# Kernel optimization log

Measured on AMD Instinct MI355X. Metric: run time of the kernel, lower is better.

Reference implementation:

```python
import jax, jax.numpy as jnp
import numpy as np

B, L, H = 4, 1024, 1024
NH, HD = 16, 64
ND = NH * HD
ITERS = 4
U = 5  # MSA1 ring window size (hard-coded in source)


def _conv1x1(w, b, x):  # w [O,C], b [O], x [B,C,L] -> [B,O,L]  (Conv2d 1x1 == per-position linear)
    return jnp.einsum('oc,bcl->bol', w, x) + b[None, :, None]


def _layernorm(x, s, b, eps=1e-5):  # x [B,H,L]; LayerNorm over channel dim H
    mu = x.mean(1, keepdims=True)
    var = ((x - mu) ** 2).mean(1, keepdims=True)
    return (x - mu) / jnp.sqrt(var + eps) * s[None, :, None] + b[None, :, None]


def _msa1(x, ax, wq, bq, wk, bk, wv, bv, wo, bo):
    # x [B,H,L] normalized nodes; ax [B,H,2,L] (ring embedding + relay)
    b, h, l = x.shape
    q = _conv1x1(wq, bq, x).reshape(b, NH, HD, l)
    k = _conv1x1(wk, bk, x).reshape(b, NH, HD, l)
    v = _conv1x1(wv, bv, x).reshape(b, NH, HD, l)
    pad = U // 2
    kp = jnp.pad(k, ((0, 0), (0, 0), (0, 0), (pad, pad)))
    vp = jnp.pad(v, ((0, 0), (0, 0), (0, 0), (pad, pad)))
    # F.unfold with (U,1) kernel along L == stack of U shifted views
    kw = jnp.stack([kp[..., u:u + l] for u in range(U)], axis=3)  # [B,NH,HD,U,L]
    vw = jnp.stack([vp[..., u:u + l] for u in range(U)], axis=3)
    al = ax.shape[2]
    ak = (jnp.einsum('oc,bcal->boal', wk, ax) + bk[None, :, None, None]).reshape(b, NH, HD, al, l)
    av = (jnp.einsum('oc,bcal->boal', wv, ax) + bv[None, :, None, None]).reshape(b, NH, HD, al, l)
    kw = jnp.concatenate([kw, ak], axis=3)  # [B,NH,HD,U+2,L]
    vw = jnp.concatenate([vw, av], axis=3)
    scores = (q[:, :, :, None, :] * kw).sum(2) / np.sqrt(HD)  # [B,NH,U+2,L]
    alphas = jax.nn.softmax(scores, axis=2)
    att = (alphas[:, :, None, :, :] * vw).sum(3).reshape(b, ND, l)
    return _conv1x1(wo, bo, att)  # [B,H,L]


def _msa2(relay, y, smask, wq, bq, wk, bk, wo, bo):
    # relay [B,H]; y [B,H,L+1]; smask [B,L+1] True at padding
    b = relay.shape[0]
    q = (jnp.einsum('oc,bc->bo', wq, relay) + bq).reshape(b, NH, HD)
    k = _conv1x1(wk, bk, y).reshape(b, NH, HD, -1)
    pre = jnp.einsum('bnd,bndl->bnl', q, k) / np.sqrt(HD)
    pre = jnp.where(smask[:, None, :], -1e10, pre)
    alphas = jax.nn.softmax(pre, axis=-1)
    # NOTE: source has v = k (WV output unused) -- reproduced faithfully
    att = jnp.einsum('bnl,bndl->bnd', alphas, k).reshape(b, ND)
    return jnp.einsum('oc,bc->bo', wo, att) + bo  # [B,H]


def _star_forward(data, mask, ln_s, ln_b, rwq, rwq_b, rwk, rwk_b, rwv, rwv_b, rwo, rwo_b,
                  swq, swq_b, swk, swk_b, swo, swo_b):
    b, l, h = data.shape
    pad_mask = (mask == 0)  # True at padding positions
    smask = jnp.concatenate([jnp.zeros((b, 1), bool), pad_mask], axis=1)  # [B,L+1]
    embs = jnp.transpose(data, (0, 2, 1))  # [B,H,L]
    nodes = embs
    relay = embs.mean(2)  # [B,H]
    for i in range(ITERS):
        xn = _layernorm(nodes, ln_s[i], ln_b[i])
        ax = jnp.stack([embs, jnp.broadcast_to(relay[:, :, None], embs.shape)], axis=2)  # [B,H,2,L]
        ring = _msa1(xn, ax, rwq[i], rwq_b[i], rwk[i], rwk_b[i], rwv[i], rwv_b[i], rwo[i], rwo_b[i])
        nodes = nodes + jax.nn.leaky_relu(ring)
        y = jnp.concatenate([relay[:, :, None], nodes], axis=2)  # [B,H,L+1]
        relay = jax.nn.leaky_relu(_msa2(relay, y, smask, swq[i], swq_b[i], swk[i], swk_b[i], swo[i], swo_b[i]))
        nodes = jnp.where(pad_mask[:, None, :], 0.0, nodes)
    return jnp.transpose(nodes, (0, 2, 1)), relay  # [B,L,H], [B,H]


def setup_inputs() -> dict:
    key = jax.random.key(0)
    ks = jax.random.split(key, 16)
    def p(k, shape):
        return jax.random.normal(k, shape, jnp.float32) * 0.02
    return dict(
        data=jax.random.normal(ks[0], (B, L, H), jnp.float32),
        mask=jax.random.randint(ks[1], (B, L), 0, 2).astype(jnp.int32),
        ln_s=jnp.ones((ITERS, H), jnp.float32),
        ln_b=jnp.zeros((ITERS, H), jnp.float32),
        rwq=p(ks[2], (ITERS, ND, H)), rwq_b=p(ks[3], (ITERS, ND)),
        rwk=p(ks[4], (ITERS, ND, H)), rwk_b=p(ks[5], (ITERS, ND)),
        rwv=p(ks[6], (ITERS, ND, H)), rwv_b=p(ks[7], (ITERS, ND)),
        rwo=p(ks[8], (ITERS, H, ND)), rwo_b=p(ks[9], (ITERS, H)),
        swq=p(ks[10], (ITERS, ND, H)), swq_b=p(ks[11], (ITERS, ND)),
        swk=p(ks[12], (ITERS, ND, H)), swk_b=p(ks[13], (ITERS, ND)),
        swo=p(ks[14], (ITERS, H, ND)), swo_b=p(ks[15], (ITERS, H)),
    )


def reference(data, mask, ln_s, ln_b, rwq, rwq_b, rwk, rwk_b, rwv, rwv_b, rwo, rwo_b,
              swq, swq_b, swk, swk_b, swo, swo_b):
    return _star_forward(data, mask, ln_s, ln_b, rwq, rwq_b, rwk, rwk_b, rwv, rwv_b,
                         rwo, rwo_b, swq, swq_b, swk, swk_b, swo, swo_b)
```

## Files before the change

kernel.cpp:

```cpp
#include <hip/hip_runtime.h>
#include <math.h>

namespace {

constexpr int B_ = 4, L_ = 1024, H_ = 1024, NH_ = 16, HD_ = 64, ND_ = 1024, ITERS_ = 4;

typedef unsigned short u16;
typedef __attribute__((ext_vector_type(8))) short short8;
typedef __attribute__((ext_vector_type(4))) float f32x4;

__device__ inline u16 f2bf(float f) {
  unsigned u = __builtin_bit_cast(unsigned, f);
  u += 0x7FFFu + ((u >> 16) & 1u);
  return (u16)(u >> 16);
}
__device__ inline float bf2f(u16 v) {
  unsigned u = ((unsigned)v) << 16;
  return __builtin_bit_cast(float, u);
}

__device__ inline void gl_lds16(const u16* g, u16* l) {
  __builtin_amdgcn_global_load_lds((const __attribute__((address_space(1))) void*)g,
                                   (__attribute__((address_space(3))) void*)l, 16, 0, 0);
}

__global__ void k_prep(const float* __restrict__ data, const float* __restrict__ rwq,
                       const float* __restrict__ rwk, const float* __restrict__ rwv,
                       const float* __restrict__ rwo, const float* __restrict__ swk,
                       u16* __restrict__ embs_bf, u16* __restrict__ wq_bf,
                       u16* __restrict__ wk_bf, u16* __restrict__ wv_bf,
                       u16* __restrict__ wo_bf, u16* __restrict__ swk_bf,
                       float* __restrict__ nodes) {
  int i = blockIdx.x * 256 + threadIdx.x;
  int which = blockIdx.y;
  if (which == 6) {
    reinterpret_cast<float4*>(nodes)[i] = reinterpret_cast<const float4*>(data)[i];
    return;
  }
  const float* src;
  u16* dst;
  switch (which) {
    case 0: src = data; dst = embs_bf; break;
    case 1: src = rwq; dst = wq_bf; break;
    case 2: src = rwk; dst = wk_bf; break;
    case 3: src = rwv; dst = wv_bf; break;
    case 4: src = rwo; dst = wo_bf; break;
    default: src = swk; dst = swk_bf; break;
  }
  float4 v = reinterpret_cast<const float4*>(src)[i];
  ushort4 o;
  o.x = f2bf(v.x); o.y = f2bf(v.y); o.z = f2bf(v.z); o.w = f2bf(v.w);
  reinterpret_cast<ushort4*>(dst)[i] = o;
}

__global__ void k_relay_part(const float* __restrict__ data, float* __restrict__ part) {
  int b = blockIdx.z, chunk = blockIdx.y;
  int c = blockIdx.x * 256 + threadIdx.x;
  const float* p = data + ((size_t)b * L_ + chunk * 128) * H_ + c;
  float acc = 0.f;
  for (int l = 0; l < 128; ++l) acc += p[(size_t)l * H_];
  part[((size_t)b * 8 + chunk) * H_ + c] = acc;
}
__global__ void k_relay_reduce(const float* __restrict__ part, float* __restrict__ relay) {
  int i = blockIdx.x * 256 + threadIdx.x;
  int b = i >> 10, c = i & 1023;
  float acc = 0.f;
  for (int j = 0; j < 8; ++j) acc += part[((size_t)b * 8 + j) * H_ + c];
  relay[i] = acc * (1.f / (float)L_);
}

__global__ __launch_bounds__(256) void k_layernorm_bf(float* __restrict__ nodes,
                                                      const float* __restrict__ s,
                                                      const float* __restrict__ bb,
                                                      const int* __restrict__ mask,
                                                      u16* __restrict__ y, int do_zero) {
  int row = blockIdx.x * 4 + (threadIdx.x >> 6);
  int lane = threadIdx.x & 63;
  int b = row >> 10, l = row & 1023;
  bool pad = do_zero && (mask[b * L_ + l] == 0);
  float4* xr = reinterpret_cast<float4*>(nodes + (size_t)row * H_);
  float4 v[4];
  float sum = 0.f, sq = 0.f;
#pragma unroll
  for (int j = 0; j < 4; ++j) {
    v[j] = pad ? float4{0.f, 0.f, 0.f, 0.f} : xr[lane + 64 * j];
    sum += v[j].x + v[j].y + v[j].z + v[j].w;
    sq += v[j].x * v[j].x + v[j].y * v[j].y + v[j].z * v[j].z + v[j].w * v[j].w;
  }
  if (pad) {
#pragma unroll
    for (int j = 0; j < 4; ++j) xr[lane + 64 * j] = float4{0.f, 0.f, 0.f, 0.f};
  }
#pragma unroll
  for (int off = 32; off; off >>= 1) {
    sum += __shfl_xor(sum, off);
    sq += __shfl_xor(sq, off);
  }
  float mu = sum * (1.f / (float)H_);
  float rstd = rsqrtf(sq * (1.f / (float)H_) - mu * mu + 1e-5f);
  ushort4* yr = reinterpret_cast<ushort4*>(y + (size_t)row * H_);
#pragma unroll
  for (int j = 0; j < 4; ++j) {
    int c4 = lane + 64 * j;
    float4 sc = reinterpret_cast<const float4*>(s)[c4];
    float4 bc = reinterpret_cast<const float4*>(bb)[c4];
    ushort4 o;
    o.x = f2bf((v[j].x - mu) * rstd * sc.x + bc.x);
    o.y = f2bf((v[j].y - mu) * rstd * sc.y + bc.y);
    o.z = f2bf((v[j].z - mu) * rstd * sc.z + bc.z);
    o.w = f2bf((v[j].w - mu) * rstd * sc.w + bc.w);
    yr[c4] = o;
  }
}

__global__ __launch_bounds__(256, 2) void k_gemm5(const u16* __restrict__ wq,
                                                  const u16* __restrict__ wk,
                                                  const u16* __restrict__ wv,
                                                  const float* __restrict__ bq,
                                                  const float* __restrict__ bk,
                                                  const float* __restrict__ bv,
                                                  const u16* __restrict__ xn,
                                                  const u16* __restrict__ embs,
                                                  u16* __restrict__ Y) {
  __shared__ __align__(16) u16 sX[2][256 * 32];
  __shared__ __align__(16) u16 sW[2][128 * 32];
  const int bm = blockIdx.x * 256;
  const int which = blockIdx.y >> 3;
  const int bn = (blockIdx.y & 7) * 128;
  const u16* W = (which == 0) ? wq : ((which == 1 || which == 3) ? wk : wv);
  const float* bias = (which == 0) ? bq : ((which == 1 || which == 3) ? bk : bv);
  const u16* X = (which < 3) ? xn : embs;
  u16* Yw = Y + (size_t)which * ((size_t)B_ * L_ * ND_);

  const int t = threadIdx.x;
  const int w = t >> 6, lane = t & 63;
  const int wo_ = w & 1, wx = w >> 1;
  const int r4 = lane >> 2, slot = lane & 3;

  const int rowW0 = w * 16 + r4, rowW1 = 64 + rowW0;
  const int colW0 = ((slot ^ ((rowW0 >> 1) & 3)) << 3);
  const int colW1 = ((slot ^ ((rowW1 >> 1) & 3)) << 3);
  const u16* gW0 = W + (size_t)(bn + rowW0) * 1024 + colW0;
  const u16* gW1 = W + (size_t)(bn + rowW1) * 1024 + colW1;
  const u16* gX0;
  const u16* gX1;
  const u16* gX2;
  const u16* gX3;
  {
    int r0 = w * 16 + r4;
    int r1 = r0 + 64, r2 = r0 + 128, r3 = r0 + 192;
    gX0 = X + (size_t)(bm + r0) * 1024 + ((slot ^ ((r0 >> 1) & 3)) << 3);
    gX1 = X + (size_t)(bm + r1) * 1024 + ((slot ^ ((r1 >> 1) & 3)) << 3);
    gX2 = X + (size_t)(bm + r2) * 1024 + ((slot ^ ((r2 >> 1) & 3)) << 3);
    gX3 = X + (size_t)(bm + r3) * 1024 + ((slot ^ ((r3 >> 1) & 3)) << 3);
  }
  const int kidx = (((lane >> 4) ^ ((lane >> 1) & 3)) << 3);
  const int rW = wo_ * 64 + (lane & 15);
  const int rX = wx * 128 + (lane & 15);

  f32x4 acc[4][8];
#pragma unroll
  for (int i_ = 0; i_ < 4; ++i_)
#pragma unroll
    for (int j_ = 0; j_ < 8; ++j_) acc[i_][j_] = f32x4{0.f, 0.f, 0.f, 0.f};

  for (int ck = 0; ck < 1024; ck += 64) {
    gl_lds16(gX0, sX[0] + w * 512);
    gl_lds16(gX0 + 32, sX[1] + w * 512);
    gl_lds16(gX1, sX[0] + w * 512 + 2048);
    gl_lds16(gX1 + 32, sX[1] + w * 512 + 2048);
    gl_lds16(gX2, sX[0] + w * 512 + 4096);
    gl_lds16(gX2 + 32, sX[1] + w * 512 + 4096);
    gl_lds16(gX3, sX[0] + w * 512 + 6144);
    gl_lds16(gX3 + 32, sX[1] + w * 512 + 6144);
    gl_lds16(gW0, sW[0] + w * 512);
    gl_lds16(gW0 + 32, sW[1] + w * 512);
    gl_lds16(gW1, sW[0] + (4 + w) * 512);
    gl_lds16(gW1 + 32, sW[1] + (4 + w) * 512);
    gX0 += 64; gX1 += 64; gX2 += 64; gX3 += 64; gW0 += 64; gW1 += 64;
    __syncthreads();
#pragma unroll
    for (int h = 0; h < 2; ++h) {
      short8 aw[4], bx[8];
#pragma unroll
      for (int mf = 0; mf < 4; ++mf)
        aw[mf] = *reinterpret_cast<const short8*>(&sW[h][(rW + mf * 16) * 32 + kidx]);
#pragma unroll
      for (int nl = 0; nl < 8; ++nl)
        bx[nl] = *reinterpret_cast<const short8*>(&sX[h][(rX + nl * 16) * 32 + kidx]);
#pragma unroll
      for (int mf = 0; mf < 4; ++mf)
#pragma unroll
        for (int nl = 0; nl < 8; ++nl)
          acc[mf][nl] = __builtin_amdgcn_mfma_f32_16x16x32_bf16(aw[mf], bx[nl], acc[mf][nl], 0, 0, 0);
    }
    __syncthreads();
  }

#pragma unroll
  for (int mo = 0; mo < 4; ++mo) {
    int o0 = bn + wo_ * 64 + mo * 16 + ((lane >> 4) << 2);
    float4 bs = *reinterpret_cast<const float4*>(bias + o0);
#pragma unroll
    for (int nl = 0; nl < 8; ++nl) {
      int bl = bm + wx * 128 + nl * 16 + (lane & 15);
      f32x4 vv = acc[mo][nl];
      ushort4 ov;
      ov.x = f2bf(vv[0] + bs.x);
      ov.y = f2bf(vv[1] + bs.y);
      ov.z = f2bf(vv[2] + bs.z);
      ov.w = f2bf(vv[3] + bs.w);
      *reinterpret_cast<ushort4*>(&Yw[(size_t)bl * 1024 + o0]) = ov;
    }
  }
}


#define SMALL_PROLOGUE(XPTR, WPTR)                                             \
  __shared__ __align__(16) u16 sX[2][128 * 32];                                \
  __shared__ __align__(16) u16 sW[2][64 * 32];                                 \
  const int t = threadIdx.x;                                                   \
  const int w = t >> 6, lane = t & 63;                                         \
  const int wm = w >> 1, wn = w & 1;                                           \
  const int r4 = lane >> 2, slot = lane & 3;                                   \
  const int rowS0 = w * 16 + r4, rowS1 = 64 + rowS0;                           \
  const int colS0 = ((slot ^ ((rowS0 >> 1) & 3)) << 3);                        \
  const int colS1 = ((slot ^ ((rowS1 >> 1) & 3)) << 3);                        \
  const u16* gX0 = (XPTR) + (size_t)(bm + rowS0) * 1024 + colS0;               \
  const u16* gX1 = (XPTR) + (size_t)(bm + rowS1) * 1024 + colS1;               \
  const u16* gW0 = (WPTR) + (size_t)(bn + rowS0) * 1024 + colS0;               \
  u16* lX0a = sX[0] + w * 512;                                                 \
  u16* lX0b = sX[1] + w * 512;                                                 \
  u16* lX1a = sX[0] + (4 + w) * 512;                                           \
  u16* lX1b = sX[1] + (4 + w) * 512;                                           \
  u16* lW0a = sW[0] + w * 512;                                                 \
  u16* lW0b = sW[1] + w * 512;                                                 \
  const int kidx = (((lane >> 4) ^ ((lane >> 1) & 3)) << 3);

#define SMALL_KLOOP(MFN, NFN, ACC, AROWBASE, BROWBASE, ASRC, BSRC)             \
  for (int ck = 0; ck < 1024; ck += 64) {                                      \
    gl_lds16(gX0, lX0a);                                                       \
    gl_lds16(gX0 + 32, lX0b);                                                  \
    gl_lds16(gX1, lX1a);                                                       \
    gl_lds16(gX1 + 32, lX1b);                                                  \
    gl_lds16(gW0, lW0a);                                                       \
    gl_lds16(gW0 + 32, lW0b);                                                  \
    gX0 += 64; gX1 += 64; gW0 += 64;                                           \
    __syncthreads();                                                           \
    _Pragma("unroll") for (int h = 0; h < 2; ++h) {                            \
      short8 af_[MFN], bf_[NFN];                                               \
      _Pragma("unroll") for (int mf = 0; mf < MFN; ++mf)                       \
          af_[mf] = *reinterpret_cast<const short8*>(                          \
              &ASRC[h][((AROWBASE) + mf * 16) * 32 + kidx]);                   \
      _Pragma("unroll") for (int nf = 0; nf < NFN; ++nf)                       \
          bf_[nf] = *reinterpret_cast<const short8*>(                          \
              &BSRC[h][((BROWBASE) + nf * 16) * 32 + kidx]);                   \
      _Pragma("unroll") for (int mf = 0; mf < MFN; ++mf)                       \
          _Pragma("unroll") for (int nf = 0; nf < NFN; ++nf)                   \
              ACC[mf][nf] = __builtin_amdgcn_mfma_f32_16x16x32_bf16(           \
                  af_[mf], bf_[nf], ACC[mf][nf], 0, 0, 0);                     \
    }                                                                          \
    __syncthreads();                                                          \
  }

__global__ __launch_bounds__(256, 2) void k_gemm_wo_s(const u16* __restrict__ W,
                                                      const float* __restrict__ bias,
                                                      const u16* __restrict__ X,
                                                      float* __restrict__ nodes,
                                                      u16* __restrict__ nodes_bf) {
  const int bm = blockIdx.x * 128;
  const int bn = blockIdx.y * 64;
  SMALL_PROLOGUE(X, W)
  f32x4 acc[2][4];
#pragma unroll
  for (int i_ = 0; i_ < 2; ++i_)
#pragma unroll
    for (int j_ = 0; j_ < 4; ++j_) acc[i_][j_] = f32x4{0.f, 0.f, 0.f, 0.f};
  const int rW = wm * 32 + (lane & 15);
  const int rX = wn * 64 + (lane & 15);
  SMALL_KLOOP(2, 4, acc, rW, rX, sW, sX)

#pragma unroll
  for (int mo = 0; mo < 2; ++mo) {
    int o0 = bn + wm * 32 + mo * 16 + ((lane >> 4) << 2);
    float4 bs = *reinterpret_cast<const float4*>(bias + o0);
#pragma unroll
    for (int nl = 0; nl < 4; ++nl) {
      int bl = bm + wn * 64 + nl * 16 + (lane & 15);
      size_t ni = (size_t)bl * 1024 + o0;
      float4 curv = *reinterpret_cast<const float4*>(&nodes[ni]);
      f32x4 vv = acc[mo][nl];
      float r0 = vv[0] + bs.x; r0 = curv.x + (r0 > 0.f ? r0 : 0.01f * r0);
      float r1 = vv[1] + bs.y; r1 = curv.y + (r1 > 0.f ? r1 : 0.01f * r1);
      float r2 = vv[2] + bs.z; r2 = curv.z + (r2 > 0.f ? r2 : 0.01f * r2);
      float r3 = vv[3] + bs.w; r3 = curv.w + (r3 > 0.f ? r3 : 0.01f * r3);
      *reinterpret_cast<float4*>(&nodes[ni]) = float4{r0, r1, r2, r3};
      ushort4 ov;
      ov.x = f2bf(r0); ov.y = f2bf(r1); ov.z = f2bf(r2); ov.w = f2bf(r3);
      *reinterpret_cast<ushort4*>(&nodes_bf[ni]) = ov;
    }
  }
}

__global__ __launch_bounds__(256, 2) void k_gemm_kkb_sw(const u16* __restrict__ W,
                                                        const float* __restrict__ bias,
                                                        const u16* __restrict__ X,
                                                        u16* __restrict__ Y) {
  const int bm = blockIdx.x * 128;
  const int bn = blockIdx.y * 64;
  SMALL_PROLOGUE(X, W)
  f32x4 acc[2][4];
#pragma unroll
  for (int i_ = 0; i_ < 2; ++i_)
#pragma unroll
    for (int j_ = 0; j_ < 4; ++j_) acc[i_][j_] = f32x4{0.f, 0.f, 0.f, 0.f};
  const int rW = wm * 32 + (lane & 15);
  const int rX = wn * 64 + (lane & 15);
  SMALL_KLOOP(2, 4, acc, rW, rX, sW, sX)

#pragma unroll
  for (int mo = 0; mo < 2; ++mo) {
    int o0 = bn + wm * 32 + mo * 16 + ((lane >> 4) << 2);
    float4 bs = *reinterpret_cast<const float4*>(bias + o0);
#pragma unroll
    for (int nl = 0; nl < 4; ++nl) {
      int bl = bm + wn * 64 + nl * 16 + (lane & 15);
      size_t row = (size_t)(bl >> 10) * 1025 + 1 + (bl & 1023);
      f32x4 vv = acc[mo][nl];
      ushort4 ov;
      ov.x = f2bf(vv[0] + bs.x);
      ov.y = f2bf(vv[1] + bs.y);
      ov.z = f2bf(vv[2] + bs.z);
      ov.w = f2bf(vv[3] + bs.w);
      *reinterpret_cast<ushort4*>(&Y[row * 1024 + o0]) = ov;
    }
  }
}

__global__ __launch_bounds__(256) void k_matvec4(const float* __restrict__ W0,
                                                 const float* __restrict__ b0, float* __restrict__ y0,
                                                 const float* __restrict__ W1,
                                                 const float* __restrict__ b1, float* __restrict__ y1,
                                                 const float* __restrict__ W2,
                                                 const float* __restrict__ b2, float* __restrict__ y2,
                                                 const float* __restrict__ W3,
                                                 const float* __restrict__ b3, u16* __restrict__ y3b,
                                                 const float* __restrict__ x) {
  int b = blockIdx.y, z = blockIdx.z;
  const float* W = (z == 0) ? W0 : (z == 1) ? W1 : (z == 2) ? W2 : W3;
  const float* bias = (z == 0) ? b0 : (z == 1) ? b1 : (z == 2) ? b2 : b3;
  int o = blockIdx.x * 4 + (threadIdx.x >> 6);
  int lane = threadIdx.x & 63;
  const float* wr = W + (size_t)o * 1024;
  const float* xb = x + (size_t)b * 1024;
  float acc = 0.f;
  for (int c = lane; c < 1024; c += 64) acc += wr[c] * xb[c];
#pragma unroll
  for (int off = 32; off; off >>= 1) acc += __shfl_xor(acc, off);
  if (lane == 0) {
    acc += bias[o];
    if (z == 3) y3b[(size_t)b * 1025 * 1024 + o] = f2bf(acc);
    else if (z == 2) y2[(size_t)b * 1024 + o] = acc;
    else if (z == 1) y1[(size_t)b * 1024 + o] = acc;
    else y0[(size_t)b * 1024 + o] = acc;
  }
}

__global__ __launch_bounds__(256) void k_matvec(const float* __restrict__ W,
                                                const float* __restrict__ bias,
                                                const float* __restrict__ x,
                                                float* __restrict__ y, int leaky) {
  int b = blockIdx.y;
  int o = blockIdx.x * 4 + (threadIdx.x >> 6);
  int lane = threadIdx.x & 63;
  const float* wr = W + (size_t)o * 1024;
  const float* xb = x + (size_t)b * 1024;
  float acc = 0.f;
  for (int c = lane; c < 1024; c += 64) acc += wr[c] * xb[c];
#pragma unroll
  for (int off = 32; off; off >>= 1) acc += __shfl_xor(acc, off);
  if (lane == 0) {
    acc += bias[o];
    if (leaky) acc = acc > 0.f ? acc : 0.01f * acc;
    y[(size_t)b * 1024 + o] = acc;
  }
}

__global__ __launch_bounds__(256) void k_msa1(const u16* __restrict__ q,
                                              const u16* __restrict__ k,
                                              const u16* __restrict__ v,
                                              const u16* __restrict__ ke,
                                              const u16* __restrict__ ve,
                                              const float* __restrict__ rk,
                                              const float* __restrict__ rv,
                                              u16* __restrict__ attbf) {
  int t = threadIdx.x;
  int wv = t >> 6, lane = t & 63;
  int head = lane >> 2, dq = lane & 3;
  int l = blockIdx.x * 4 + wv;
  int b = blockIdx.z;
  size_t row = ((size_t)(b * 1024 + l)) * 1024 + head * 64 + dq * 16;
  size_t rbase = (size_t)b * 1024 + head * 64 + dq * 16;

  float qf[16];
  {
    const short8* qp = reinterpret_cast<const short8*>(q + row);
#pragma unroll
    for (int j = 0; j < 2; ++j) {
      short8 qv = qp[j];
#pragma unroll
      for (int e = 0; e < 8; ++e) qf[j * 8 + e] = bf2f((u16)qv[e]);
    }
  }
  float s[7];
#pragma unroll
  for (int u = 0; u < 5; ++u) {
    int lk = l + u - 2;
    float su = 0.f;
    if (lk >= 0 && lk < L_) {
      const short8* kp = reinterpret_cast<const short8*>(
          k + ((size_t)(b * 1024 + lk)) * 1024 + head * 64 + dq * 16);
#pragma unroll
      for (int j = 0; j < 2; ++j) {
        short8 kv = kp[j];
#pragma unroll
        for (int e = 0; e < 8; ++e) su = fmaf(qf[j * 8 + e], bf2f((u16)kv[e]), su);
      }
    }
    s[u] = su;
  }
  {
    float su = 0.f;
    const short8* kp = reinterpret_cast<const short8*>(ke + row);
#pragma unroll
    for (int j = 0; j < 2; ++j) {
      short8 kv = kp[j];
#pragma unroll
      for (int e = 0; e < 8; ++e) su = fmaf(qf[j * 8 + e], bf2f((u16)kv[e]), su);
    }
    s[5] = su;
  }
  {
    float su = 0.f;
    const float4* rp = reinterpret_cast<const float4*>(rk + rbase);
#pragma unroll
    for (int j = 0; j < 4; ++j) {
      float4 r4 = rp[j];
      su = fmaf(qf[j * 4 + 0], r4.x, su);
      su = fmaf(qf[j * 4 + 1], r4.y, su);
      su = fmaf(qf[j * 4 + 2], r4.z, su);
      su = fmaf(qf[j * 4 + 3], r4.w, su);
    }
    s[6] = su;
  }
#pragma unroll
  for (int u = 0; u < 7; ++u) {
    s[u] += __shfl_xor(s[u], 1);
    s[u] += __shfl_xor(s[u], 2);
  }
  float m = -1e30f;
#pragma unroll
  for (int u = 0; u < 7; ++u) {
    s[u] *= 0.125f;
    m = fmaxf(m, s[u]);
  }
  float e[7], tot = 0.f;
#pragma unroll
  for (int u = 0; u < 7; ++u) {
    e[u] = expf(s[u] - m);
    tot += e[u];
  }
  float inv = 1.f / tot;
#pragma unroll
  for (int u = 0; u < 7; ++u) e[u] *= inv;

  float av[16];
  {
    const float4* rp = reinterpret_cast<const float4*>(rv + rbase);
#pragma unroll
    for (int j = 0; j < 4; ++j) {
      float4 r4 = rp[j];
      av[j * 4 + 0] = e[6] * r4.x;
      av[j * 4 + 1] = e[6] * r4.y;
      av[j * 4 + 2] = e[6] * r4.z;
      av[j * 4 + 3] = e[6] * r4.w;
    }
  }
  {
    const short8* vp = reinterpret_cast<const short8*>(ve + row);
#pragma unroll
    for (int j = 0; j < 2; ++j) {
      short8 vvv = vp[j];
#pragma unroll
      for (int ee = 0; ee < 8; ++ee) av[j * 8 + ee] = fmaf(e[5], bf2f((u16)vvv[ee]), av[j * 8 + ee]);
    }
  }
#pragma unroll
  for (int u = 0; u < 5; ++u) {
    int lk = l + u - 2;
    if (lk >= 0 && lk < L_) {
      const short8* vp = reinterpret_cast<const short8*>(
          v + ((size_t)(b * 1024 + lk)) * 1024 + head * 64 + dq * 16);
#pragma unroll
      for (int j = 0; j < 2; ++j) {
        short8 vvv = vp[j];
#pragma unroll
        for (int ee = 0; ee < 8; ++ee) av[j * 8 + ee] = fmaf(e[u], bf2f((u16)vvv[ee]), av[j * 8 + ee]);
      }
    }
  }
  u16 ob[16];
#pragma unroll
  for (int j = 0; j < 16; ++j) ob[j] = f2bf(av[j]);
  uint4* d4 = reinterpret_cast<uint4*>(attbf + row);
  const uint4* s4 = reinterpret_cast<const uint4*>(ob);
  d4[0] = s4[0];
  d4[1] = s4[1];
}

__global__ __launch_bounds__(256) void k_msa2f(const u16* __restrict__ kkb,
                                               const float* __restrict__ rq,
                                               const int* __restrict__ mask,
                                               float* __restrict__ avp,
                                               float* __restrict__ Ep) {
  int b = blockIdx.y;
  int w = threadIdx.x >> 6, lane = threadIdx.x & 63;
  int wc = blockIdx.x * 4 + w;
  int q4 = lane & 3;
  int ch0 = lane * 16;
  float rqv[16];
  {
    const float4* rp = reinterpret_cast<const float4*>(rq + (size_t)b * 1024 + ch0);
#pragma unroll
    for (int j = 0; j < 4; ++j) {
      float4 v4 = rp[j];
      rqv[j * 4 + 0] = v4.x; rqv[j * 4 + 1] = v4.y;
      rqv[j * 4 + 2] = v4.z; rqv[j * 4 + 3] = v4.w;
    }
  }
  float av[16];
#pragma unroll
  for (int j = 0; j < 16; ++j) av[j] = 0.f;
  float eacc = 0.f;
  int p0 = wc * 16;
  int pend = p0 + 16;
  if (pend > 1025) pend = 1025;
  for (int p = p0; p < pend; ++p) {
    if (p > 0 && mask[b * L_ + p - 1] == 0) continue;
    const uint4* kr = reinterpret_cast<const uint4*>(kkb + ((size_t)b * 1025 + p) * 1024 + ch0);
    uint4 ka = kr[0], kb2 = kr[1];
    float kf[16];
    const u16* kp = reinterpret_cast<const u16*>(&ka);
#pragma unroll
    for (int j = 0; j < 8; ++j) kf[j] = bf2f(kp[j]);
    const u16* kp2 = reinterpret_cast<const u16*>(&kb2);
#pragma unroll
    for (int j = 0; j < 8; ++j) kf[8 + j] = bf2f(kp2[j]);
    float s = 0.f;
#pragma unroll
    for (int j = 0; j < 16; ++j) s = fmaf(rqv[j], kf[j], s);
    s += __shfl_xor(s, 1);
    s += __shfl_xor(s, 2);
    float e = expf(s * 0.125f);
    if (q4 == 0) eacc += e;
#pragma unroll
    for (int j = 0; j < 16; ++j) av[j] = fmaf(e, kf[j], av[j]);
  }
  float* ap = avp + ((size_t)b * 68 + wc) * 1024 + ch0;
#pragma unroll
  for (int j = 0; j < 4; ++j)
    reinterpret_cast<float4*>(ap)[j] =
        float4{av[j * 4 + 0], av[j * 4 + 1], av[j * 4 + 2], av[j * 4 + 3]};
  if (q4 == 0) Ep[((size_t)b * 68 + wc) * 16 + (lane >> 2)] = eacc;
}

__global__ void k_msa2r(const float* __restrict__ avp, const float* __restrict__ Ep,
                        float* __restrict__ satt) {
  int b = blockIdx.y;
  int idx = blockIdx.x * 256 + threadIdx.x;
  int head = idx >> 6;
  float a = 0.f, E = 0.f;
  for (int k = 0; k < 68; ++k) a += avp[((size_t)b * 68 + k) * 1024 + idx];
  for (int k = 0; k < 68; ++k) E += Ep[((size_t)b * 68 + k) * 16 + head];
  satt[(size_t)b * 1024 + idx] = a / E;
}

__global__ void k_final(const float* __restrict__ nodes, const int* __restrict__ mask,
                        float* __restrict__ out) {
  int i = blockIdx.x * 256 + threadIdx.x;
  int row = i >> 8;
  int b = row >> 10, l = row & 1023;
  float4 v = (mask[b * L_ + l] == 0) ? float4{0.f, 0.f, 0.f, 0.f}
                                     : reinterpret_cast<const float4*>(nodes)[i];
  reinterpret_cast<float4*>(out)[i] = v;
}

__global__ void k_copy_relay(const float* __restrict__ relay, float* __restrict__ out) {
  int i = blockIdx.x * 256 + threadIdx.x;
  out[i] = relay[i];
}

}

extern "C" void kernel_launch(void* const* d_in, const int* in_sizes, int n_in,
                              void* d_out, int out_size, void* d_ws, size_t ws_size,
                              hipStream_t stream) {
  (void)in_sizes; (void)n_in; (void)out_size; (void)ws_size;
  const float* data = (const float*)d_in[0];
  const int* mask = (const int*)d_in[1];
  const float* ln_s = (const float*)d_in[2];
  const float* ln_b = (const float*)d_in[3];
  const float* rwq = (const float*)d_in[4];
  const float* rwq_b = (const float*)d_in[5];
  const float* rwk = (const float*)d_in[6];
  const float* rwk_b = (const float*)d_in[7];
  const float* rwv = (const float*)d_in[8];
  const float* rwv_b = (const float*)d_in[9];
  const float* rwo = (const float*)d_in[10];
  const float* rwo_b = (const float*)d_in[11];
  const float* swq = (const float*)d_in[12];
  const float* swq_b = (const float*)d_in[13];
  const float* swk = (const float*)d_in[14];
  const float* swk_b = (const float*)d_in[15];
  const float* swo = (const float*)d_in[16];
  const float* swo_b = (const float*)d_in[17];
  float* out = (float*)d_out;

  const size_t SZ = (size_t)B_ * ND_ * L_;
  float* f = (float*)d_ws;
  float* nodes = f; f += SZ;
  float* part = f; f += (size_t)B_ * 8 * H_;
  float* relay = f; f += B_ * H_;
  float* rk = f; f += B_ * ND_;
  float* rv = f; f += B_ * ND_;
  float* rq = f; f += B_ * ND_;
  float* satt = f; f += B_ * ND_;
  float* avp = f; f += (size_t)B_ * 68 * 1024;
  float* Ep = f; f += (size_t)B_ * 68 * 16;
  u16* u = (u16*)f;
  u16* xn_bf = u; u += SZ;
  u16* embs_bf = u; u += SZ;
  u16* att_bf = u; u += SZ;
  u16* nodes_bf = u; u += SZ;
  u16* kkb_sw = u; u += (size_t)B_ * 1025 * 1024;
  u16* qkv5_bf = u; u += 5 * SZ;
  u16* wq_bf = u; u += SZ;
  u16* wk_bf = u; u += SZ;
  u16* wv_bf = u; u += SZ;
  u16* wo_bf = u; u += SZ;
  u16* swk_bf = u; u += SZ;

  k_prep<<<dim3(4096, 7), 256, 0, stream>>>(data, rwq, rwk, rwv, rwo, swk,
                                            embs_bf, wq_bf, wk_bf, wv_bf, wo_bf, swk_bf, nodes);
  k_relay_part<<<dim3(H_ / 256, 8, B_), 256, 0, stream>>>(data, part);
  k_relay_reduce<<<dim3((B_ * H_) / 256), 256, 0, stream>>>(part, relay);

  for (int i = 0; i < ITERS_; ++i) {
    const u16* wq_i = wq_bf + (size_t)i * ND_ * H_;
    const u16* wk_i = wk_bf + (size_t)i * ND_ * H_;
    const u16* wv_i = wv_bf + (size_t)i * ND_ * H_;
    const u16* wo_i = wo_bf + (size_t)i * H_ * ND_;
    const u16* sk_i = swk_bf + (size_t)i * ND_ * H_;

    k_layernorm_bf<<<dim3(B_ * L_ / 4), 256, 0, stream>>>(nodes, ln_s + i * H_, ln_b + i * H_,
                                                          mask, xn_bf, i > 0 ? 1 : 0);
    k_matvec4<<<dim3(256, B_, 4), 256, 0, stream>>>(
        rwk + (size_t)i * ND_ * H_, rwk_b + i * ND_, rk,
        rwv + (size_t)i * ND_ * H_, rwv_b + i * ND_, rv,
        swq + (size_t)i * ND_ * H_, swq_b + i * ND_, rq,
        swk + (size_t)i * ND_ * H_, swk_b + i * ND_, kkb_sw, relay);
    k_gemm5<<<dim3(16, 40), 256, 0, stream>>>(wq_i, wk_i, wv_i,
                                              rwq_b + i * ND_, rwk_b + i * ND_, rwv_b + i * ND_,
                                              xn_bf, embs_bf, qkv5_bf);
    k_msa1<<<dim3(L_ / 4, 1, B_), 256, 0, stream>>>(qkv5_bf, qkv5_bf + SZ, qkv5_bf + 2 * SZ,
                                                    qkv5_bf + 3 * SZ, qkv5_bf + 4 * SZ, rk, rv, att_bf);
    k_gemm_wo_s<<<dim3(32, 16), 256, 0, stream>>>(wo_i, rwo_b + i * H_, att_bf, nodes, nodes_bf);
    k_gemm_kkb_sw<<<dim3(32, 16), 256, 0, stream>>>(sk_i, swk_b + i * ND_, nodes_bf, kkb_sw);
    k_msa2f<<<dim3(17, B_), 256, 0, stream>>>(kkb_sw, rq, mask, avp, Ep);
    k_msa2r<<<dim3(4, B_), 256, 0, stream>>>(avp, Ep, satt);
    k_matvec<<<dim3(256, B_), 256, 0, stream>>>(swo + (size_t)i * H_ * ND_, swo_b + i * H_,
                                                satt, relay, 1);
  }
  k_final<<<4096, 256, 0, stream>>>(nodes, mask, out);
  k_copy_relay<<<dim3((B_ * H_) / 256), 256, 0, stream>>>(relay, out + (size_t)B_ * L_ * H_);
}
```

Before: 676.9 us.

## Load GEMM weight fragments directly from global into registers, shrink gemm5 tile

The three bf16 GEMM kernels stop staging the weight operand through LDS. Each wave now loads its MFMA A-fragments straight from global memory into registers, so only the activation tile goes through LDS. k_gemm5's tile shrinks from 256x128 to 128x128, doubling its grid, and launch bounds rise to 3 blocks per CU to raise occupancy. The risk is that weight reads from global lose the LDS sharing across waves, costing more global or L2 traffic and exposing load latency before the MFMAs.

```diff
diff --git a/kernel.cpp b/kernel.cpp
--- a/kernel.cpp
+++ b/kernel.cpp
@@ -113,7 +113,8 @@
   }
 }
 
-__global__ __launch_bounds__(256, 2) void k_gemm5(const u16* __restrict__ wq,
+
+__global__ __launch_bounds__(256, 3) void k_gemm5(const u16* __restrict__ wq,
                                                   const u16* __restrict__ wk,
                                                   const u16* __restrict__ wv,
                                                   const float* __restrict__ bq,
@@ -122,9 +123,8 @@
                                                   const u16* __restrict__ xn,
                                                   const u16* __restrict__ embs,
                                                   u16* __restrict__ Y) {
-  __shared__ __align__(16) u16 sX[2][256 * 32];
-  __shared__ __align__(16) u16 sW[2][128 * 32];
-  const int bm = blockIdx.x * 256;
+  __shared__ __align__(16) u16 sX[2][128 * 32];
+  const int bm = blockIdx.x * 128;
   const int which = blockIdx.y >> 3;
   const int bn = (blockIdx.y & 7) * 128;
   const u16* W = (which == 0) ? wq : ((which == 1 || which == 3) ? wk : wv);
@@ -134,76 +134,63 @@
 
   const int t = threadIdx.x;
   const int w = t >> 6, lane = t & 63;
-  const int wo_ = w & 1, wx = w >> 1;
+  const int wm = w >> 1, wn = w & 1;
   const int r4 = lane >> 2, slot = lane & 3;
-
-  const int rowW0 = w * 16 + r4, rowW1 = 64 + rowW0;
-  const int colW0 = ((slot ^ ((rowW0 >> 1) & 3)) << 3);
-  const int colW1 = ((slot ^ ((rowW1 >> 1) & 3)) << 3);
-  const u16* gW0 = W + (size_t)(bn + rowW0) * 1024 + colW0;
-  const u16* gW1 = W + (size_t)(bn + rowW1) * 1024 + colW1;
-  const u16* gX0;
-  const u16* gX1;
-  const u16* gX2;
-  const u16* gX3;
-  {
-    int r0 = w * 16 + r4;
-    int r1 = r0 + 64, r2 = r0 + 128, r3 = r0 + 192;
-    gX0 = X + (size_t)(bm + r0) * 1024 + ((slot ^ ((r0 >> 1) & 3)) << 3);
-    gX1 = X + (size_t)(bm + r1) * 1024 + ((slot ^ ((r1 >> 1) & 3)) << 3);
-    gX2 = X + (size_t)(bm + r2) * 1024 + ((slot ^ ((r2 >> 1) & 3)) << 3);
-    gX3 = X + (size_t)(bm + r3) * 1024 + ((slot ^ ((r3 >> 1) & 3)) << 3);
-  }
+  const int rowS0 = w * 16 + r4, rowS1 = 64 + rowS0;
+  const int colS0 = ((slot ^ ((rowS0 >> 1) & 3)) << 3);
+  const int colS1 = ((slot ^ ((rowS1 >> 1) & 3)) << 3);
+  const u16* gX0 = X + (size_t)(bm + rowS0) * 1024 + colS0;
+  const u16* gX1 = X + (size_t)(bm + rowS1) * 1024 + colS1;
   const int kidx = (((lane >> 4) ^ ((lane >> 1) & 3)) << 3);
-  const int rW = wo_ * 64 + (lane & 15);
-  const int rX = wx * 128 + (lane & 15);
-
-  f32x4 acc[4][8];
+  const int rX = wn * 64 + (lane & 15);
+  const u16* gWf[4];
+#pragma unroll
+  for (int mf = 0; mf < 4; ++mf)
+    gWf[mf] = W + (size_t)(bn + wm * 64 + mf * 16 + (lane & 15)) * 1024 + ((lane >> 4) << 3);
+
+  f32x4 acc[4][4];
 #pragma unroll
   for (int i_ = 0; i_ < 4; ++i_)
 #pragma unroll
-    for (int j_ = 0; j_ < 8; ++j_) acc[i_][j_] = f32x4{0.f, 0.f, 0.f, 0.f};
+    for (int j_ = 0; j_ < 4; ++j_) acc[i_][j_] = f32x4{0.f, 0.f, 0.f, 0.f};
 
   for (int ck = 0; ck < 1024; ck += 64) {
     gl_lds16(gX0, sX[0] + w * 512);
     gl_lds16(gX0 + 32, sX[1] + w * 512);
-    gl_lds16(gX1, sX[0] + w * 512 + 2048);
-    gl_lds16(gX1 + 32, sX[1] + w * 512 + 2048);
-    gl_lds16(gX2, sX[0] + w * 512 + 4096);
-    gl_lds16(gX2 + 32, sX[1] + w * 512 + 4096);
-    gl_lds16(gX3, sX[0] + w * 512 + 6144);
-    gl_lds16(gX3 + 32, sX[1] + w * 512 + 6144);
-    gl_lds16(gW0, sW[0] + w * 512);
-    gl_lds16(gW0 + 32, sW[1] + w * 512);
-    gl_lds16(gW1, sW[0] + (4 + w) * 512);
-    gl_lds16(gW1 + 32, sW[1] + (4 + w) * 512);
-    gX0 += 64; gX1 += 64; gX2 += 64; gX3 += 64; gW0 += 64; gW1 += 64;
+    gl_lds16(gX1, sX[0] + (4 + w) * 512);
+    gl_lds16(gX1 + 32, sX[1] + (4 + w) * 512);
+    gX0 += 64; gX1 += 64;
+    short8 wf[2][4];
+#pragma unroll
+    for (int h = 0; h < 2; ++h)
+#pragma unroll
+      for (int mf = 0; mf < 4; ++mf)
+        wf[h][mf] = *reinterpret_cast<const short8*>(gWf[mf] + h * 32);
+#pragma unroll
+    for (int mf = 0; mf < 4; ++mf) gWf[mf] += 64;
     __syncthreads();
 #pragma unroll
     for (int h = 0; h < 2; ++h) {
-      short8 aw[4], bx[8];
+      short8 bx[4];
+#pragma unroll
+      for (int nf = 0; nf < 4; ++nf)
+        bx[nf] = *reinterpret_cast<const short8*>(&sX[h][(rX + nf * 16) * 32 + kidx]);
 #pragma unroll
       for (int mf = 0; mf < 4; ++mf)
-        aw[mf] = *reinterpret_cast<const short8*>(&sW[h][(rW + mf * 16) * 32 + kidx]);
-#pragma unroll
-      for (int nl = 0; nl < 8; ++nl)
-        bx[nl] = *reinterpret_cast<const short8*>(&sX[h][(rX + nl * 16) * 32 + kidx]);
-#pragma unroll
-      for (int mf = 0; mf < 4; ++mf)
-#pragma unroll
-        for (int nl = 0; nl < 8; ++nl)
-          acc[mf][nl] = __builtin_amdgcn_mfma_f32_16x16x32_bf16(aw[mf], bx[nl], acc[mf][nl], 0, 0, 0);
+#pragma unroll
+        for (int nf = 0; nf < 4; ++nf)
+          acc[mf][nf] = __builtin_amdgcn_mfma_f32_16x16x32_bf16(wf[h][mf], bx[nf], acc[mf][nf], 0, 0, 0);
     }
     __syncthreads();
   }
 
 #pragma unroll
   for (int mo = 0; mo < 4; ++mo) {
-    int o0 = bn + wo_ * 64 + mo * 16 + ((lane >> 4) << 2);
+    int o0 = bn + wm * 64 + mo * 16 + ((lane >> 4) << 2);
     float4 bs = *reinterpret_cast<const float4*>(bias + o0);
 #pragma unroll
-    for (int nl = 0; nl < 8; ++nl) {
-      int bl = bm + wx * 128 + nl * 16 + (lane & 15);
+    for (int nl = 0; nl < 4; ++nl) {
+      int bl = bm + wn * 64 + nl * 16 + (lane & 15);
       f32x4 vv = acc[mo][nl];
       ushort4 ov;
       ov.x = f2bf(vv[0] + bs.x);
@@ -218,7 +205,6 @@
 
 #define SMALL_PROLOGUE(XPTR, WPTR)                                             \
   __shared__ __align__(16) u16 sX[2][128 * 32];                                \
-  __shared__ __align__(16) u16 sW[2][64 * 32];                                 \
   const int t = threadIdx.x;                                                   \
   const int w = t >> 6, lane = t & 63;                                         \
   const int wm = w >> 1, wn = w & 1;                                           \
@@ -228,42 +214,44 @@
   const int colS1 = ((slot ^ ((rowS1 >> 1) & 3)) << 3);                        \
   const u16* gX0 = (XPTR) + (size_t)(bm + rowS0) * 1024 + colS0;               \
   const u16* gX1 = (XPTR) + (size_t)(bm + rowS1) * 1024 + colS1;               \
-  const u16* gW0 = (WPTR) + (size_t)(bn + rowS0) * 1024 + colS0;               \
-  u16* lX0a = sX[0] + w * 512;                                                 \
-  u16* lX0b = sX[1] + w * 512;                                                 \
-  u16* lX1a = sX[0] + (4 + w) * 512;                                           \
-  u16* lX1b = sX[1] + (4 + w) * 512;                                           \
-  u16* lW0a = sW[0] + w * 512;                                                 \
-  u16* lW0b = sW[1] + w * 512;                                                 \
-  const int kidx = (((lane >> 4) ^ ((lane >> 1) & 3)) << 3);
-
-#define SMALL_KLOOP(MFN, NFN, ACC, AROWBASE, BROWBASE, ASRC, BSRC)             \
+  const int kidx = (((lane >> 4) ^ ((lane >> 1) & 3)) << 3);                   \
+  const int rX = wn * 64 + (lane & 15);                                        \
+  const u16* gWf[2];                                                           \
+  _Pragma("unroll") for (int mf = 0; mf < 2; ++mf)                             \
+      gWf[mf] = (WPTR) + (size_t)(bn + wm * 32 + mf * 16 + (lane & 15)) * 1024 \
+                + ((lane >> 4) << 3);                                          \
+  f32x4 acc[2][4];                                                             \
+  _Pragma("unroll") for (int i_ = 0; i_ < 2; ++i_)                             \
+      _Pragma("unroll") for (int j_ = 0; j_ < 4; ++j_)                         \
+          acc[i_][j_] = f32x4{0.f, 0.f, 0.f, 0.f};
+
+#define SMALL_KLOOP()                                                          \
   for (int ck = 0; ck < 1024; ck += 64) {                                      \
-    gl_lds16(gX0, lX0a);                                                       \
-    gl_lds16(gX0 + 32, lX0b);                                                  \
-    gl_lds16(gX1, lX1a);                                                       \
-    gl_lds16(gX1 + 32, lX1b);                                                  \
-    gl_lds16(gW0, lW0a);                                                       \
-    gl_lds16(gW0 + 32, lW0b);                                                  \
-    gX0 += 64; gX1 += 64; gW0 += 64;                                           \
+    gl_lds16(gX0, sX[0] + w * 512);                                            \
+    gl_lds16(gX0 + 32, sX[1] + w * 512);                                       \
+    gl_lds16(gX1, sX[0] + (4 + w) * 512);                                      \
+    gl_lds16(gX1 + 32, sX[1] + (4 + w) * 512);                                 \
+    gX0 += 64; gX1 += 64;                                                      \
+    short8 wf[2][2];                                                           \
+    _Pragma("unroll") for (int h = 0; h < 2; ++h)                              \
+        _Pragma("unroll") for (int mf = 0; mf < 2; ++mf)                       \
+            wf[h][mf] = *reinterpret_cast<const short8*>(gWf[mf] + h * 32);    \
+    _Pragma("unroll") for (int mf = 0; mf < 2; ++mf) gWf[mf] += 64;            \
     __syncthreads();                                                           \
     _Pragma("unroll") for (int h = 0; h < 2; ++h) {                            \
-      short8 af_[MFN], bf_[NFN];                                               \
-      _Pragma("unroll") for (int mf = 0; mf < MFN; ++mf)                       \
-          af_[mf] = *reinterpret_cast<const short8*>(                          \
-              &ASRC[h][((AROWBASE) + mf * 16) * 32 + kidx]);                   \
-      _Pragma("unroll") for (int nf = 0; nf < NFN; ++nf)                       \
-          bf_[nf] = *reinterpret_cast<const short8*>(                          \
-              &BSRC[h][((BROWBASE) + nf * 16) * 32 + kidx]);                   \
-      _Pragma("unroll") for (int mf = 0; mf < MFN; ++mf)                       \
-          _Pragma("unroll") for (int nf = 0; nf < NFN; ++nf)                   \
-              ACC[mf][nf] = __builtin_amdgcn_mfma_f32_16x16x32_bf16(           \
-                  af_[mf], bf_[nf], ACC[mf][nf], 0, 0, 0);                     \
+      short8 bx[4];                                                            \
+      _Pragma("unroll") for (int nf = 0; nf < 4; ++nf)                         \
+          bx[nf] = *reinterpret_cast<const short8*>(                           \
+              &sX[h][(rX + nf * 16) * 32 + kidx]);                             \
+      _Pragma("unroll") for (int mf = 0; mf < 2; ++mf)                         \
+          _Pragma("unroll") for (int nf = 0; nf < 4; ++nf)                     \
+              acc[mf][nf] = __builtin_amdgcn_mfma_f32_16x16x32_bf16(           \
+                  wf[h][mf], bx[nf], acc[mf][nf], 0, 0, 0);                    \
     }                                                                          \
     __syncthreads();                                                          \
   }
 
-__global__ __launch_bounds__(256, 2) void k_gemm_wo_s(const u16* __restrict__ W,
+__global__ __launch_bounds__(256, 3) void k_gemm_wo_s(const u16* __restrict__ W,
                                                       const float* __restrict__ bias,
                                                       const u16* __restrict__ X,
                                                       float* __restrict__ nodes,
@@ -271,14 +259,7 @@
   const int bm = blockIdx.x * 128;
   const int bn = blockIdx.y * 64;
   SMALL_PROLOGUE(X, W)
-  f32x4 acc[2][4];
-#pragma unroll
-  for (int i_ = 0; i_ < 2; ++i_)
-#pragma unroll
-    for (int j_ = 0; j_ < 4; ++j_) acc[i_][j_] = f32x4{0.f, 0.f, 0.f, 0.f};
-  const int rW = wm * 32 + (lane & 15);
-  const int rX = wn * 64 + (lane & 15);
-  SMALL_KLOOP(2, 4, acc, rW, rX, sW, sX)
+  SMALL_KLOOP()
 
 #pragma unroll
   for (int mo = 0; mo < 2; ++mo) {
@@ -302,21 +283,14 @@
   }
 }
 
-__global__ __launch_bounds__(256, 2) void k_gemm_kkb_sw(const u16* __restrict__ W,
+__global__ __launch_bounds__(256, 3) void k_gemm_kkb_sw(const u16* __restrict__ W,
                                                         const float* __restrict__ bias,
                                                         const u16* __restrict__ X,
                                                         u16* __restrict__ Y) {
   const int bm = blockIdx.x * 128;
   const int bn = blockIdx.y * 64;
   SMALL_PROLOGUE(X, W)
-  f32x4 acc[2][4];
-#pragma unroll
-  for (int i_ = 0; i_ < 2; ++i_)
-#pragma unroll
-    for (int j_ = 0; j_ < 4; ++j_) acc[i_][j_] = f32x4{0.f, 0.f, 0.f, 0.f};
-  const int rW = wm * 32 + (lane & 15);
-  const int rX = wn * 64 + (lane & 15);
-  SMALL_KLOOP(2, 4, acc, rW, rX, sW, sX)
+  SMALL_KLOOP()
 
 #pragma unroll
   for (int mo = 0; mo < 2; ++mo) {
@@ -669,7 +643,7 @@
         rwv + (size_t)i * ND_ * H_, rwv_b + i * ND_, rv,
         swq + (size_t)i * ND_ * H_, swq_b + i * ND_, rq,
         swk + (size_t)i * ND_ * H_, swk_b + i * ND_, kkb_sw, relay);
-    k_gemm5<<<dim3(16, 40), 256, 0, stream>>>(wq_i, wk_i, wv_i,
+    k_gemm5<<<dim3(32, 40), 256, 0, stream>>>(wq_i, wk_i, wv_i,
                                               rwq_b + i * ND_, rwk_b + i * ND_, rwv_b + i * ND_,
                                               xn_bf, embs_bf, qkv5_bf);
     k_msa1<<<dim3(L_ / 4, 1, B_), 256, 0, stream>>>(qkv5_bf, qkv5_bf + SZ, qkv5_bf + 2 * SZ,
```

Result: slower. 866.5 us (+28.0%).
